# Performance work log

Measured on AMD Instinct MI355X. Metric: run time of the kernel, lower is better.

Reference implementation:

```python
import jax, jax.numpy as jnp
import numpy as np

B, L, D, H, P = 4, 4096, 1024, 8, 4
DPH = D // H


def _grid_sample_row(v, grid):
    """F.grid_sample for a (N, C, 1, Lv) input, bilinear, padding_mode='zeros',
    align_corners=False. v: (N, C, Lv), grid: (N, Lq, P, 2) with (x, y) in last dim.
    Returns (N, C, Lq, P)."""
    N, C, Lv = v.shape
    x = grid[..., 0]
    y = grid[..., 1]
    # unnormalize (align_corners=False): u = ((coord + 1) * size - 1) / 2
    ux = ((x + 1.0) * Lv - 1.0) * 0.5          # width = Lv
    uy = ((y + 1.0) * 1.0 - 1.0) * 0.5         # height = 1
    x0f = jnp.floor(ux)
    wx1 = ux - x0f
    wx0 = 1.0 - wx1
    y0f = jnp.floor(uy)
    wy1 = uy - y0f
    wy0 = 1.0 - wy1
    # only row 0 exists; rows outside contribute zero (padding zeros)
    wy = wy0 * (y0f == 0.0) + wy1 * ((y0f + 1.0) == 0.0)   # (N, Lq, P)
    i0 = x0f.astype(jnp.int32)
    i1 = i0 + 1
    m0 = (i0 >= 0) & (i0 < Lv)
    m1 = (i1 >= 0) & (i1 < Lv)
    i0c = jnp.clip(i0, 0, Lv - 1)
    i1c = jnp.clip(i1, 0, Lv - 1)
    # gather along width per batch element: (C, Lv)[:, (Lq, P)] -> (C, Lq, P)
    v0 = jax.vmap(lambda vv, ii: vv[:, ii])(v, i0c)
    v1 = jax.vmap(lambda vv, ii: vv[:, ii])(v, i1c)
    w0 = (wx0 * m0 * wy)[:, None, :, :]
    w1 = (wx1 * m1 * wy)[:, None, :, :]
    return v0 * w0 + v1 * w1


def setup_inputs() -> dict:
    key = jax.random.key(0)
    ks = jax.random.split(key, 16)
    s = 0.02
    f32 = jnp.float32
    return {
        "query": jax.random.normal(ks[0], (B, L, D), f32),
        "key_in": jax.random.normal(ks[1], (B, L, D), f32),
        "value": jax.random.normal(ks[2], (B, L, D), f32),
        "Wqk": jax.random.normal(ks[3], (D, 2 * D), f32) * s,
        "bqk": jnp.zeros((2 * D,), f32),
        "Wv": jax.random.normal(ks[4], (D, D), f32) * s,
        "bv": jnp.zeros((D,), f32),
        "Woff": jax.random.normal(ks[5], (D, H * P * 2), f32) * s,
        "boff": jax.random.normal(ks[6], (H * P * 2,), f32) * 0.25,
        "Wattn": jax.random.normal(ks[7], (D, H * P), f32) * s,
        "battn": jnp.zeros((H * P,), f32),
        "Wo": jax.random.normal(ks[8], (D, D), f32) * s,
        "bo": jnp.zeros((D,), f32),
    }


def reference(query, key_in, value, Wqk, bqk, Wv, bv, Woff, boff, Wattn, battn, Wo, bo):
    # qk_proj: q, k are computed in the original but never used downstream (dead code)
    qk = query @ Wqk + bqk
    q, k = jnp.split(qk, 2, axis=-1)  # noqa: unused, matches original

    v = value @ Wv + bv                                   # (B, L, D)

    # reference points: x base = linspace[0] = 0, y base = i/(L-1) for query i
    ref_y = jnp.linspace(0.0, 1.0, L)
    ref = jnp.stack([jnp.zeros_like(ref_y), ref_y], axis=-1)   # (L, 2)

    offsets = (query @ Woff + boff).reshape(B, L, H, P, 2)
    attn = jax.nn.softmax((query @ Wattn + battn).reshape(B, L, H, P), axis=-1)

    loc = jnp.clip(ref[None, :, None, None, :] + offsets, 0.0, 1.0)  # (B, L, H, P, 2)

    # value -> (B*H, dph, L)
    vh = v.reshape(B, L, H, DPH).transpose(0, 2, 3, 1).reshape(B * H, DPH, L)
    grid = loc.transpose(0, 2, 1, 3, 4).reshape(B * H, L, P, 2)

    sampled = _grid_sample_row(vh, grid)                  # (B*H, dph, L, P)
    sampled = sampled.reshape(B, H, DPH, L, P)

    aw = attn.transpose(0, 2, 1, 3)[:, :, None, :, :]     # (B, H, 1, L, P)
    out = (sampled * aw).sum(-1)                          # (B, H, dph, L)
    out = out.transpose(0, 3, 1, 2).reshape(B, L, D)
    return out @ Wo + bo
```

## Files before the change

kernel.cpp:

```cpp
#include <hip/hip_runtime.h>

#define L_Q 4096
#define D_MODEL 1024
#define N_B 4
#define N_H 8
#define N_P 4
#define M_ROWS (N_B * L_Q)

typedef float f32x4 __attribute__((ext_vector_type(4)));
typedef __bf16 bf16x8 __attribute__((ext_vector_type(8)));
typedef unsigned short u16x8 __attribute__((ext_vector_type(8)));

__device__ __forceinline__ unsigned short f2bf(float f) {
    unsigned int u = __float_as_uint(f);
    u += 0x7FFFu + ((u >> 16) & 1u);
    return (unsigned short)(u >> 16);
}
__device__ __forceinline__ float bf2f(unsigned short s) {
    return __uint_as_float(((unsigned int)s) << 16);
}

__device__ __forceinline__ void gload_lds16(const void* g, void* l) {
    __builtin_amdgcn_global_load_lds((const __attribute__((address_space(1))) void*)g,
                                     (__attribute__((address_space(3))) void*)l,
                                     16, 0, 0);
}

template <int N> __device__ __forceinline__ void wait_vmc() {
    if constexpr (N == 5)      asm volatile("s_waitcnt vmcnt(5)"  ::: "memory");
    else if constexpr (N == 4) asm volatile("s_waitcnt vmcnt(4)"  ::: "memory");
    else                       asm volatile("s_waitcnt vmcnt(0)"  ::: "memory");
}

#define RAW_BAR() asm volatile("s_barrier" ::: "memory")


__global__ void k_prep(const float* __restrict__ Wv, const float* __restrict__ Wo,
                       const float* __restrict__ Woff, const float* __restrict__ Wattn,
                       const float* __restrict__ value,
                       unsigned short* __restrict__ WvT, unsigned short* __restrict__ WoT,
                       unsigned short* __restrict__ WcT2, unsigned short* __restrict__ val_bf) {
    __shared__ float tile[64 * 65];
    const int bidx = blockIdx.x;
    const int t = threadIdx.x;

    if (bidx < 512) {
        const float* W = (bidx < 256) ? Wv : Wo;
        unsigned short* WT = (bidx < 256) ? WvT : WoT;
        const int bi = bidx & 255;
        const int k0 = (bi >> 4) * 64, n0 = (bi & 15) * 64;
#pragma unroll
        for (int j = 0; j < 4; ++j) {
            const int r = j * 16 + (t >> 4);
            float4 v = *(const float4*)(W + (size_t)(k0 + r) * 1024 + n0 + (t & 15) * 4);
            float* d = &tile[r * 65 + (t & 15) * 4];
            d[0] = v.x; d[1] = v.y; d[2] = v.z; d[3] = v.w;
        }
        __syncthreads();
#pragma unroll
        for (int j = 0; j < 4; ++j) {
            const int n = j * 16 + (t >> 4);
            const int kc = (t & 15) * 4;
            ushort4 o;
            o.x = f2bf(tile[(kc + 0) * 65 + n]);
            o.y = f2bf(tile[(kc + 1) * 65 + n]);
            o.z = f2bf(tile[(kc + 2) * 65 + n]);
            o.w = f2bf(tile[(kc + 3) * 65 + n]);
            *(ushort4*)(WT + (size_t)(n0 + n) * 1024 + k0 + kc) = o;
        }
    } else if (bidx < 544) {
        const int bi = bidx - 512;
        const int k0 = (bi >> 1) * 64;
        const int ntile = bi & 1;
        const int n0 = ntile * 64;
        const int nw = ntile ? 32 : 64;
        const int ldw = ntile ? 32 : 64;
        const float* W = ntile ? Wattn : Woff;
#pragma unroll
        for (int j = 0; j < 4; ++j) {
            const int r = j * 16 + (t >> 4);
            const int c4 = t & 15;
            if (c4 * 4 < nw) {
                float4 v = *(const float4*)(W + (size_t)(k0 + r) * ldw + c4 * 4);
                float* d = &tile[r * 65 + c4 * 4];
                d[0] = v.x; d[1] = v.y; d[2] = v.z; d[3] = v.w;
            }
        }
        __syncthreads();
#pragma unroll
        for (int j = 0; j < 4; ++j) {
            const int n = j * 16 + (t >> 4);
            if (n < nw) {
                const int kc = (t & 15) * 4;
                ushort4 hi, lo;
                float f0 = tile[(kc + 0) * 65 + n];
                float f1 = tile[(kc + 1) * 65 + n];
                float f2 = tile[(kc + 2) * 65 + n];
                float f3 = tile[(kc + 3) * 65 + n];
                hi.x = f2bf(f0); lo.x = f2bf(f0 - bf2f(hi.x));
                hi.y = f2bf(f1); lo.y = f2bf(f1 - bf2f(hi.y));
                hi.z = f2bf(f2); lo.z = f2bf(f2 - bf2f(hi.z));
                hi.w = f2bf(f3); lo.w = f2bf(f3 - bf2f(hi.w));
                const size_t base = (size_t)(n0 + n) * 2048 + k0 + kc;
                *(ushort4*)(WcT2 + base) = hi;
                *(ushort4*)(WcT2 + base + 1024) = lo;
            }
        }
    } else {
        const int n8 = M_ROWS * D_MODEL / 8;
        int i = (bidx - 544) * 256 + t;
        const int stride = (gridDim.x - 544) * 256;
        for (; i < n8; i += stride) {
            float4 a = ((const float4*)value)[2 * i];
            float4 b = ((const float4*)value)[2 * i + 1];
            u16x8 o;
            o[0] = f2bf(a.x); o[1] = f2bf(a.y); o[2] = f2bf(a.z); o[3] = f2bf(a.w);
            o[4] = f2bf(b.x); o[5] = f2bf(b.y); o[6] = f2bf(b.z); o[7] = f2bf(b.w);
            ((u16x8*)val_bf)[i] = o;
        }
    }
}


template <bool OUT_BF16>
__global__ __launch_bounds__(512, 2) void k_gemm256(const unsigned short* __restrict__ A,
                                                    const unsigned short* __restrict__ Bt,
                                                    const float* __restrict__ bias,
                                                    void* __restrict__ Cout) {
    __shared__ __align__(16) unsigned short lds[2][2][2][8192];
    const int tid = threadIdx.x;
    const int w = tid >> 6, lane = tid & 63;
    const int wm = w >> 2, wn = w & 3;

    const int bid = blockIdx.x;
    const int swz = (bid & 7) * 32 + (bid >> 3);
    const int m0 = (swz >> 2) * 256;
    const int n0 = (swz & 3) * 256;

    const int sr = (w << 3) + (lane >> 3);
    const int sc = (lane & 7) ^ ((lane >> 3) & 7);
    const size_t aoff1 = (size_t)(m0 + sr) * 1024 + (size_t)(sc * 8);
    const size_t boff1 = (size_t)(n0 + sr) * 1024 + (size_t)(sc * 8);

    const int fr = lane & 15, kq = lane >> 4;
    const int cs0 = ((kq) ^ (fr & 7)) * 8;
    const int cs1 = ((4 + kq) ^ (fr & 7)) * 8;
    const int arow = (wm * 64 + fr) * 64;
    const int brow = (wn * 32 + fr) * 64;

    f32x4 acc[2][2][4][2];
    const f32x4 zero = {0.f, 0.f, 0.f, 0.f};
#pragma unroll
    for (int qm = 0; qm < 2; ++qm)
#pragma unroll
        for (int qn = 0; qn < 2; ++qn)
#pragma unroll
            for (int i = 0; i < 4; ++i)
#pragma unroll
                for (int j = 0; j < 2; ++j) acc[qm][qn][i][j] = zero;

    bf16x8 af[4][2], bl[2][2], bh[2][2];

#define GSTA(set, half, kt) do {                                                        \
        const unsigned short* g_ = A + aoff1 + (size_t)(half) * 131072 + (size_t)(kt);  \
        unsigned short* d_ = &lds[0][set][half][0] + w * 512;                           \
        gload_lds16(g_, d_);                                                            \
        gload_lds16(g_ + 65536, d_ + 4096);                                             \
    } while (0)

#define GSTB(set, half, kt) do {                                                        \
        const unsigned short* g_ = Bt + boff1 + (size_t)(half) * 131072 + (size_t)(kt); \
        unsigned short* d_ = &lds[1][set][half][0] + w * 512;                           \
        gload_lds16(g_, d_);                                                            \
        gload_lds16(g_ + 65536, d_ + 4096);                                             \
    } while (0)

#define MFMA1(qm, qn, i, j, kk, B_)                                                     \
    acc[qm][qn][i][j] = __builtin_amdgcn_mfma_f32_16x16x32_bf16(                        \
        af[i][kk], B_[j][kk], acc[qm][qn][i][j], 0, 0, 0)

#define LDB4(dst, set, half) do {                                                       \
        const unsigned short* sB_ = &lds[1][set][half][0];                              \
        _Pragma("unroll") for (int j = 0; j < 2; ++j) {                                 \
            dst[j][0] = *(const bf16x8*)(sB_ + brow + j * 1024 + cs0);                  \
            dst[j][1] = *(const bf16x8*)(sB_ + brow + j * 1024 + cs1);                  \
        }                                                                               \
    } while (0)

#define LDA8(set, half) do {                                                            \
        const unsigned short* sA_ = &lds[0][set][half][0];                              \
        _Pragma("unroll") for (int i = 0; i < 4; ++i) {                                 \
            af[i][0] = *(const bf16x8*)(sA_ + arow + i * 1024 + cs0);                   \
            af[i][1] = *(const bf16x8*)(sA_ + arow + i * 1024 + cs1);                   \
        }                                                                               \
    } while (0)

#define MM16(qm, qn, B_) do {                                                           \
        _Pragma("unroll") for (int i = 0; i < 4; ++i) {                                 \
            MFMA1(qm, qn, i, 0, 0, B_); MFMA1(qm, qn, i, 0, 1, B_);                     \
            MFMA1(qm, qn, i, 1, 0, B_); MFMA1(qm, qn, i, 1, 1, B_);                     \
        }                                                                               \
    } while (0)

#define MM16_LDA(qm, qn, B_, setA, halfA) do {                                          \
        const unsigned short* sA_ = &lds[0][setA][halfA][0];                            \
        _Pragma("unroll") for (int i = 0; i < 4; ++i) {                                 \
            MFMA1(qm, qn, i, 0, 0, B_); MFMA1(qm, qn, i, 0, 1, B_);                     \
            MFMA1(qm, qn, i, 1, 0, B_); MFMA1(qm, qn, i, 1, 1, B_);                     \
            af[i][0] = *(const bf16x8*)(sA_ + arow + i * 1024 + cs0);                   \
            af[i][1] = *(const bf16x8*)(sA_ + arow + i * 1024 + cs1);                   \
        }                                                                               \
    } while (0)

#define SGB_MFMA(n) __builtin_amdgcn_sched_group_barrier(0x0008, n, 0)
#define SGB_DSR(n)  __builtin_amdgcn_sched_group_barrier(0x0100, n, 0)
#define PIN_A() do { SGB_DSR(4); SGB_MFMA(16); } while (0)
#define PIN_B() do { SGB_MFMA(4); SGB_DSR(2); SGB_MFMA(4); SGB_DSR(2);                  \
                     SGB_MFMA(4); SGB_DSR(2); SGB_MFMA(4); SGB_DSR(2); } while (0)
#define PIN_D() do { SGB_DSR(4); PIN_B(); } while (0)

    GSTA(0, 0, 0);
    GSTB(0, 0, 0);
    GSTB(0, 1, 0);
    GSTA(0, 1, 0);
    wait_vmc<4>();
    RAW_BAR();
    LDA8(0, 0); LDB4(bl, 0, 0);

#pragma unroll 1
    for (int it = 0; it < 8; ++it) {
        const int kt = it * 128;
        const int ktn = (kt + 128) & 1023;
        GSTA(1, 0, kt + 64);
        wait_vmc<4>(); RAW_BAR();
        __builtin_amdgcn_s_setprio(1);
        LDB4(bh, 0, 1);
        MM16(0, 0, bl);
        PIN_A();
        __builtin_amdgcn_s_setprio(0);
        GSTB(1, 0, kt + 64);
        wait_vmc<4>(); RAW_BAR();
        __builtin_amdgcn_s_setprio(1);
        MM16_LDA(0, 1, bh, 0, 1);
        PIN_B();
        __builtin_amdgcn_s_setprio(0);
        GSTB(1, 1, kt + 64);
        RAW_BAR();
        __builtin_amdgcn_s_setprio(1);
        MM16(1, 1, bh);
        __builtin_amdgcn_s_setprio(0);
        GSTA(1, 1, kt + 64);
        wait_vmc<4>(); RAW_BAR();
        __builtin_amdgcn_s_setprio(1);
        LDB4(bh, 1, 0);
        MM16_LDA(1, 0, bl, 1, 0);
        PIN_D();
        __builtin_amdgcn_s_setprio(0);
        GSTA(0, 0, ktn);
        wait_vmc<4>(); RAW_BAR();
        __builtin_amdgcn_s_setprio(1);
        LDB4(bl, 1, 1);
        MM16(0, 0, bh);
        PIN_A();
        __builtin_amdgcn_s_setprio(0);
        GSTB(0, 0, ktn);
        wait_vmc<4>(); RAW_BAR();
        __builtin_amdgcn_s_setprio(1);
        MM16_LDA(0, 1, bl, 1, 1);
        PIN_B();
        __builtin_amdgcn_s_setprio(0);
        GSTB(0, 1, ktn);
        RAW_BAR();
        __builtin_amdgcn_s_setprio(1);
        MM16(1, 1, bl);
        __builtin_amdgcn_s_setprio(0);
        GSTA(0, 1, ktn);
        wait_vmc<4>(); RAW_BAR();
        __builtin_amdgcn_s_setprio(1);
        LDB4(bl, 0, 0);
        MM16_LDA(1, 0, bh, 0, 0);
        PIN_D();
        __builtin_amdgcn_s_setprio(0);
    }
    wait_vmc<0>();

#undef GSTA
#undef GSTB
#undef MFMA1
#undef LDB4
#undef LDA8
#undef MM16
#undef MM16_LDA
#undef SGB_MFMA
#undef SGB_DSR
#undef PIN_A
#undef PIN_B
#undef PIN_D

#pragma unroll
    for (int qm = 0; qm < 2; ++qm) {
#pragma unroll
        for (int qn = 0; qn < 2; ++qn) {
#pragma unroll
            for (int i = 0; i < 4; ++i) {
#pragma unroll
                for (int j = 0; j < 2; ++j) {
                    const int col = n0 + qn * 128 + wn * 32 + j * 16 + fr;
                    const float bcol = bias[col];
#pragma unroll
                    for (int r = 0; r < 4; ++r) {
                        const int row = m0 + qm * 128 + wm * 64 + i * 16 + kq * 4 + r;
                        const float v = acc[qm][qn][i][j][r] + bcol;
                        if (OUT_BF16)
                            ((unsigned short*)Cout)[(size_t)row * D_MODEL + col] = f2bf(v);
                        else
                            ((float*)Cout)[(size_t)row * D_MODEL + col] = v;
                    }
                }
            }
        }
    }
}


__global__ __launch_bounds__(512, 2) void k_offattn2(const float* __restrict__ query,
                                                     const unsigned short* __restrict__ WcT2,
                                                     const float* __restrict__ boff,
                                                     const float* __restrict__ battn,
                                                     float* __restrict__ C96) {
    __shared__ __align__(16) unsigned short ldsA[2][128 * 64];
    __shared__ __align__(16) unsigned short ldsB[2][192 * 64];
    const int tid = threadIdx.x;
    const int w = tid >> 6, lane = tid & 63;
    const int wm = w >> 1, wn = w & 1;
    const int m0 = blockIdx.x * 64;

    const int ar = tid >> 3;
    const int ac = tid & 7;
    const float* qbase = query + (size_t)(m0 + ar) * 1024 + ac * 8;
    const int aw_hi = ar * 64 + ((ac ^ (ar & 7)) * 8);
    const int aw_lo = (64 + ar) * 64 + ((ac ^ (ar & 7)) * 8);

    const int brl = lane >> 3;
    const int bchk = (lane & 7) ^ (brl & 7);

    const int fr = lane & 15, kq = lane >> 4;
    const int cs0 = ((kq) ^ (fr & 7)) * 8;
    const int cs1 = ((4 + kq) ^ (fr & 7)) * 8;
    const int ahr = (wm * 16 + fr) * 64;
    const int alr = (64 + wm * 16 + fr) * 64;

    f32x4 acc[3];
    const f32x4 zero = {0.f, 0.f, 0.f, 0.f};
#pragma unroll
    for (int j = 0; j < 3; ++j) acc[j] = zero;

#define ALOAD(f0_, f1_, kt_) do {                                                       \
        f0_ = *(const float4*)(qbase + (kt_));                                          \
        f1_ = *(const float4*)(qbase + (kt_) + 4);                                      \
    } while (0)

#define BSTAGE(p_, kt_) do {                                                            \
        _Pragma("unroll") for (int i_ = 0; i_ < 3; ++i_) {                              \
            const int sr_ = i_ * 64 + w * 8 + brl;                                      \
            const unsigned short* g_ = WcT2 + ((sr_ < 96)                               \
                    ? ((size_t)sr_ * 2048 + (size_t)(kt_))                              \
                    : ((size_t)(sr_ - 96) * 2048 + 1024 + (size_t)(kt_)))               \
                    + (size_t)(bchk * 8);                                               \
            gload_lds16(g_, &ldsB[p_][(i_ * 64 + w * 8) * 64]);                         \
        }                                                                               \
    } while (0)

#define AWRITE2(p_, f0_, f1_) do {                                                      \
        u16x8 hi_, lo_;                                                                 \
        const float vv_[8] = {f0_.x, f0_.y, f0_.z, f0_.w, f1_.x, f1_.y, f1_.z, f1_.w};  \
        _Pragma("unroll") for (int e_ = 0; e_ < 8; ++e_) {                              \
            hi_[e_] = f2bf(vv_[e_]);                                                    \
            lo_[e_] = f2bf(vv_[e_] - bf2f(hi_[e_]));                                    \
        }                                                                               \
        *(u16x8*)(&ldsA[p_][aw_hi]) = hi_;                                              \
        *(u16x8*)(&ldsA[p_][aw_lo]) = lo_;                                              \
    } while (0)

#define OMM(p_) do {                                                                    \
        const unsigned short* As_ = &ldsA[p_][0];                                       \
        const unsigned short* Bs_ = &ldsB[p_][0];                                       \
        bf16x8 ah0 = *(const bf16x8*)(As_ + ahr + cs0);                                 \
        bf16x8 ah1 = *(const bf16x8*)(As_ + ahr + cs1);                                 \
        bf16x8 al0 = *(const bf16x8*)(As_ + alr + cs0);                                 \
        bf16x8 al1 = *(const bf16x8*)(As_ + alr + cs1);                                 \
        __builtin_amdgcn_s_setprio(1);                                                  \
        _Pragma("unroll") for (int j = 0; j < 3; ++j) {                                 \
            const int br_ = (wn * 48 + j * 16 + fr) * 64;                               \
            bf16x8 wh0 = *(const bf16x8*)(Bs_ + br_ + cs0);                             \
            bf16x8 wh1 = *(const bf16x8*)(Bs_ + br_ + cs1);                             \
            bf16x8 wl0 = *(const bf16x8*)(Bs_ + 6144 + br_ + cs0);                      \
            bf16x8 wl1 = *(const bf16x8*)(Bs_ + 6144 + br_ + cs1);                      \
            acc[j] = __builtin_amdgcn_mfma_f32_16x16x32_bf16(ah0, wh0, acc[j], 0, 0, 0);\
            acc[j] = __builtin_amdgcn_mfma_f32_16x16x32_bf16(ah1, wh1, acc[j], 0, 0, 0);\
            acc[j] = __builtin_amdgcn_mfma_f32_16x16x32_bf16(ah0, wl0, acc[j], 0, 0, 0);\
            acc[j] = __builtin_amdgcn_mfma_f32_16x16x32_bf16(ah1, wl1, acc[j], 0, 0, 0);\
            acc[j] = __builtin_amdgcn_mfma_f32_16x16x32_bf16(al0, wh0, acc[j], 0, 0, 0);\
            acc[j] = __builtin_amdgcn_mfma_f32_16x16x32_bf16(al1, wh1, acc[j], 0, 0, 0);\
        }                                                                               \
        __builtin_amdgcn_s_setprio(0);                                                  \
    } while (0)

#define OBODY(t_, p_, fc0_, fc1_, fn0_, fn1_) do {                                      \
        if ((t_) < 15) {                                                                \
            ALOAD(fn0_, fn1_, ((t_) + 1) * 64);                                         \
            BSTAGE((p_) ^ 1, ((t_) + 1) * 64);                                          \
            wait_vmc<5>();                                                              \
        } else {                                                                        \
            wait_vmc<0>();                                                              \
        }                                                                               \
        AWRITE2(p_, fc0_, fc1_);                                                        \
        asm volatile("s_waitcnt lgkmcnt(0)" ::: "memory");                              \
        RAW_BAR();                                                                      \
        OMM(p_);                                                                        \
        RAW_BAR();                                                                      \
    } while (0)

    float4 a0A, a1A, a0B, a1B;
    ALOAD(a0A, a1A, 0);
    BSTAGE(0, 0);

#pragma unroll 1
    for (int t2 = 0; t2 < 8; ++t2) {
        const int t = t2 * 2;
        OBODY(t,     0, a0A, a1A, a0B, a1B);
        OBODY(t + 1, 1, a0B, a1B, a0A, a1A);
    }

#undef ALOAD
#undef BSTAGE
#undef AWRITE2
#undef OMM
#undef OBODY

#pragma unroll
    for (int j = 0; j < 3; ++j) {
        const int col = wn * 48 + j * 16 + fr;
        const float bcol = (col < 64) ? boff[col] : battn[col - 64];
#pragma unroll
        for (int r = 0; r < 4; ++r) {
            const int row = m0 + wm * 16 + kq * 4 + r;
            C96[(size_t)row * 96 + col] = acc[j][r] + bcol;
        }
    }
}


__global__ void k_sampler(const float* __restrict__ C96,
                          const unsigned short* __restrict__ vproj,
                          unsigned short* __restrict__ agg) {
    const int row = blockIdx.x;
    const int b = row >> 12;
    const int l = row & (L_Q - 1);
    const int t = threadIdx.x;

    __shared__ float cv[96];
    if (t < 96) cv[t] = C96[(size_t)row * 96 + t];
    __syncthreads();

    const int h = t >> 5;
    const int dd = (t & 31) * 4;
    const float ref_y = (float)l / 4095.0f;

    float lg[4];
#pragma unroll
    for (int p = 0; p < 4; ++p) lg[p] = cv[64 + h * 4 + p];
    const float mx = fmaxf(fmaxf(lg[0], lg[1]), fmaxf(lg[2], lg[3]));
    float ex[4];
    float es = 0.f;
#pragma unroll
    for (int p = 0; p < 4; ++p) { ex[p] = expf(lg[p] - mx); es += ex[p]; }
    const float inv = 1.0f / es;

    float acc0 = 0.f, acc1 = 0.f, acc2 = 0.f, acc3 = 0.f;
#pragma unroll
    for (int p = 0; p < 4; ++p) {
        const float ox = cv[h * 8 + p * 2];
        const float oy = cv[h * 8 + p * 2 + 1];
        const float lx = fminf(fmaxf(ox, 0.0f), 1.0f);
        const float ly = fminf(fmaxf(ref_y + oy, 0.0f), 1.0f);
        const float ux = (lx + 1.0f) * 2048.0f - 0.5f;
        const float wy = 1.0f - ly * 0.5f;
        const float x0f = floorf(ux);
        const int i0 = (int)x0f;
        const int i1 = i0 + 1;
        const float w1 = ux - x0f;
        const float w0 = 1.0f - w1;
        const float aw = ex[p] * inv * wy;
        const float f0 = aw * w0 * ((i0 >= 0 && i0 < L_Q) ? 1.0f : 0.0f);
        const float f1 = aw * w1 * ((i1 >= 0 && i1 < L_Q) ? 1.0f : 0.0f);
        const int i0c = i0 < 0 ? 0 : (i0 > L_Q - 1 ? L_Q - 1 : i0);
        const int i1c = i1 < 0 ? 0 : (i1 > L_Q - 1 ? L_Q - 1 : i1);
        const ushort4 v0 = *(const ushort4*)(vproj + (size_t)(b * L_Q + i0c) * D_MODEL + h * 128 + dd);
        const ushort4 v1 = *(const ushort4*)(vproj + (size_t)(b * L_Q + i1c) * D_MODEL + h * 128 + dd);
        acc0 += f0 * bf2f(v0.x) + f1 * bf2f(v1.x);
        acc1 += f0 * bf2f(v0.y) + f1 * bf2f(v1.y);
        acc2 += f0 * bf2f(v0.z) + f1 * bf2f(v1.z);
        acc3 += f0 * bf2f(v0.w) + f1 * bf2f(v1.w);
    }
    ushort4 o;
    o.x = f2bf(acc0); o.y = f2bf(acc1); o.z = f2bf(acc2); o.w = f2bf(acc3);
    *(ushort4*)(agg + (size_t)row * D_MODEL + t * 4) = o;
}


extern "C" void kernel_launch(void* const* d_in, const int* in_sizes, int n_in,
                              void* d_out, int out_size, void* d_ws, size_t ws_size,
                              hipStream_t stream) {
    const float* query = (const float*)d_in[0];
    const float* value = (const float*)d_in[2];
    const float* Wv    = (const float*)d_in[5];
    const float* bv    = (const float*)d_in[6];
    const float* Woff  = (const float*)d_in[7];
    const float* boff  = (const float*)d_in[8];
    const float* Wattn = (const float*)d_in[9];
    const float* battn = (const float*)d_in[10];
    const float* Wo    = (const float*)d_in[11];
    const float* bo    = (const float*)d_in[12];

    char* ws = (char*)d_ws;
    size_t off = 0;
    auto alloc = [&](size_t bytes) -> char* {
        char* p = ws + off;
        off += (bytes + 255) & ~(size_t)255;
        return p;
    };
    unsigned short* val_bf = (unsigned short*)alloc((size_t)M_ROWS * D_MODEL * 2);
    unsigned short* vproj  = (unsigned short*)alloc((size_t)M_ROWS * D_MODEL * 2);
    unsigned short* agg    = (unsigned short*)alloc((size_t)M_ROWS * D_MODEL * 2);
    float*          C96    = (float*)alloc((size_t)M_ROWS * 96 * 4);
    unsigned short* WvT    = (unsigned short*)alloc((size_t)D_MODEL * D_MODEL * 2);
    unsigned short* WoT    = (unsigned short*)alloc((size_t)D_MODEL * D_MODEL * 2);
    unsigned short* WcT2   = (unsigned short*)alloc((size_t)96 * 2048 * 2);

    k_prep<<<2048, 256, 0, stream>>>(Wv, Wo, Woff, Wattn, value, WvT, WoT, WcT2, val_bf);

    k_gemm256<true><<<256, 512, 0, stream>>>(val_bf, WvT, bv, vproj);

    k_offattn2<<<M_ROWS / 64, 512, 0, stream>>>(query, WcT2, boff, battn, C96);

    k_sampler<<<M_ROWS, 256, 0, stream>>>(C96, vproj, agg);

    k_gemm256<false><<<256, 512, 0, stream>>>(agg, WoT, bo, (float*)d_out);
}
```

Before: 142.8 us.

## Fuse offset/attention projection with bilinear sampler via shared memory

Merges the offset/attention-logit GEMM kernel and the sampler kernel into one. The 96-column projection results stay in LDS instead of going through a global C96 buffer, and each 512-thread block then samples its 64 rows in a loop. This removes one kernel launch and the global write and read of the intermediate. The cost is that the sampling phase now runs inside a heavier GEMM block with higher LDS use, so fewer sampler blocks are resident to hide gather latency.

```diff
diff --git a/kernel.cpp b/kernel.cpp
--- a/kernel.cpp
+++ b/kernel.cpp
@@ -323,11 +323,12 @@
 }
 
 
-__global__ __launch_bounds__(512, 2) void k_offattn2(const float* __restrict__ query,
-                                                     const unsigned short* __restrict__ WcT2,
-                                                     const float* __restrict__ boff,
-                                                     const float* __restrict__ battn,
-                                                     float* __restrict__ C96) {
+__global__ __launch_bounds__(512, 2) void k_offsamp(const float* __restrict__ query,
+                                                    const unsigned short* __restrict__ WcT2,
+                                                    const float* __restrict__ boff,
+                                                    const float* __restrict__ battn,
+                                                    const unsigned short* __restrict__ vproj,
+                                                    unsigned short* __restrict__ agg) {
     __shared__ __align__(16) unsigned short ldsA[2][128 * 64];
     __shared__ __align__(16) unsigned short ldsB[2][192 * 64];
     const int tid = threadIdx.x;
@@ -438,74 +439,74 @@
 #undef OMM
 #undef OBODY
 
+    asm volatile("s_waitcnt lgkmcnt(0)" ::: "memory");
+    __syncthreads();
+
+    float* cvs = (float*)&ldsA[0][0];
 #pragma unroll
     for (int j = 0; j < 3; ++j) {
         const int col = wn * 48 + j * 16 + fr;
         const float bcol = (col < 64) ? boff[col] : battn[col - 64];
 #pragma unroll
         for (int r = 0; r < 4; ++r) {
-            const int row = m0 + wm * 16 + kq * 4 + r;
-            C96[(size_t)row * 96 + col] = acc[j][r] + bcol;
+            const int rl = wm * 16 + kq * 4 + r;
+            cvs[rl * 96 + col] = acc[j][r] + bcol;
         }
     }
-}
-
-
-__global__ void k_sampler(const float* __restrict__ C96,
-                          const unsigned short* __restrict__ vproj,
-                          unsigned short* __restrict__ agg) {
-    const int row = blockIdx.x;
-    const int b = row >> 12;
-    const int l = row & (L_Q - 1);
-    const int t = threadIdx.x;
-
-    __shared__ float cv[96];
-    if (t < 96) cv[t] = C96[(size_t)row * 96 + t];
     __syncthreads();
 
-    const int h = t >> 5;
-    const int dd = (t & 31) * 4;
-    const float ref_y = (float)l / 4095.0f;
-
-    float lg[4];
-#pragma unroll
-    for (int p = 0; p < 4; ++p) lg[p] = cv[64 + h * 4 + p];
-    const float mx = fmaxf(fmaxf(lg[0], lg[1]), fmaxf(lg[2], lg[3]));
-    float ex[4];
-    float es = 0.f;
-#pragma unroll
-    for (int p = 0; p < 4; ++p) { ex[p] = expf(lg[p] - mx); es += ex[p]; }
-    const float inv = 1.0f / es;
-
-    float acc0 = 0.f, acc1 = 0.f, acc2 = 0.f, acc3 = 0.f;
-#pragma unroll
-    for (int p = 0; p < 4; ++p) {
-        const float ox = cv[h * 8 + p * 2];
-        const float oy = cv[h * 8 + p * 2 + 1];
-        const float lx = fminf(fmaxf(ox, 0.0f), 1.0f);
-        const float ly = fminf(fmaxf(ref_y + oy, 0.0f), 1.0f);
-        const float ux = (lx + 1.0f) * 2048.0f - 0.5f;
-        const float wy = 1.0f - ly * 0.5f;
-        const float x0f = floorf(ux);
-        const int i0 = (int)x0f;
-        const int i1 = i0 + 1;
-        const float w1 = ux - x0f;
-        const float w0 = 1.0f - w1;
-        const float aw = ex[p] * inv * wy;
-        const float f0 = aw * w0 * ((i0 >= 0 && i0 < L_Q) ? 1.0f : 0.0f);
-        const float f1 = aw * w1 * ((i1 >= 0 && i1 < L_Q) ? 1.0f : 0.0f);
-        const int i0c = i0 < 0 ? 0 : (i0 > L_Q - 1 ? L_Q - 1 : i0);
-        const int i1c = i1 < 0 ? 0 : (i1 > L_Q - 1 ? L_Q - 1 : i1);
-        const ushort4 v0 = *(const ushort4*)(vproj + (size_t)(b * L_Q + i0c) * D_MODEL + h * 128 + dd);
-        const ushort4 v1 = *(const ushort4*)(vproj + (size_t)(b * L_Q + i1c) * D_MODEL + h * 128 + dd);
-        acc0 += f0 * bf2f(v0.x) + f1 * bf2f(v1.x);
-        acc1 += f0 * bf2f(v0.y) + f1 * bf2f(v1.y);
-        acc2 += f0 * bf2f(v0.z) + f1 * bf2f(v1.z);
-        acc3 += f0 * bf2f(v0.w) + f1 * bf2f(v1.w);
+    const int b = m0 >> 12;
+#pragma unroll 2
+    for (int rep = 0; rep < 32; ++rep) {
+        const int task = rep * 512 + tid;
+        const int rl = task >> 8;
+        const int ct = task & 255;
+        const int l = (m0 + rl) & (L_Q - 1);
+        const int h = ct >> 5;
+        const int dd = (ct & 31) * 4;
+        const float ref_y = (float)l / 4095.0f;
+        const float* cv = &cvs[rl * 96];
+
+        float lg[4];
+#pragma unroll
+        for (int p = 0; p < 4; ++p) lg[p] = cv[64 + h * 4 + p];
+        const float mx = fmaxf(fmaxf(lg[0], lg[1]), fmaxf(lg[2], lg[3]));
+        float ex[4];
+        float es = 0.f;
+#pragma unroll
+        for (int p = 0; p < 4; ++p) { ex[p] = expf(lg[p] - mx); es += ex[p]; }
+        const float inv = 1.0f / es;
+
+        float acc0 = 0.f, acc1 = 0.f, acc2 = 0.f, acc3 = 0.f;
+#pragma unroll
+        for (int p = 0; p < 4; ++p) {
+            const float ox = cv[h * 8 + p * 2];
+            const float oy = cv[h * 8 + p * 2 + 1];
+            const float lx = fminf(fmaxf(ox, 0.0f), 1.0f);
+            const float ly = fminf(fmaxf(ref_y + oy, 0.0f), 1.0f);
+            const float ux = (lx + 1.0f) * 2048.0f - 0.5f;
+            const float wy = 1.0f - ly * 0.5f;
+            const float x0f = floorf(ux);
+            const int i0 = (int)x0f;
+            const int i1 = i0 + 1;
+            const float w1 = ux - x0f;
+            const float w0 = 1.0f - w1;
+            const float aw = ex[p] * inv * wy;
+            const float f0 = aw * w0 * ((i0 >= 0 && i0 < L_Q) ? 1.0f : 0.0f);
+            const float f1 = aw * w1 * ((i1 >= 0 && i1 < L_Q) ? 1.0f : 0.0f);
+            const int i0c = i0 < 0 ? 0 : (i0 > L_Q - 1 ? L_Q - 1 : i0);
+            const int i1c = i1 < 0 ? 0 : (i1 > L_Q - 1 ? L_Q - 1 : i1);
+            const ushort4 v0 = *(const ushort4*)(vproj + (size_t)(b * L_Q + i0c) * D_MODEL + h * 128 + dd);
+            const ushort4 v1 = *(const ushort4*)(vproj + (size_t)(b * L_Q + i1c) * D_MODEL + h * 128 + dd);
+            acc0 += f0 * bf2f(v0.x) + f1 * bf2f(v1.x);
+            acc1 += f0 * bf2f(v0.y) + f1 * bf2f(v1.y);
+            acc2 += f0 * bf2f(v0.z) + f1 * bf2f(v1.z);
+            acc3 += f0 * bf2f(v0.w) + f1 * bf2f(v1.w);
+        }
+        ushort4 o;
+        o.x = f2bf(acc0); o.y = f2bf(acc1); o.z = f2bf(acc2); o.w = f2bf(acc3);
+        *(ushort4*)(agg + (size_t)(m0 + rl) * D_MODEL + ct * 4) = o;
     }
-    ushort4 o;
-    o.x = f2bf(acc0); o.y = f2bf(acc1); o.z = f2bf(acc2); o.w = f2bf(acc3);
-    *(ushort4*)(agg + (size_t)row * D_MODEL + t * 4) = o;
 }
 
 
@@ -533,7 +534,6 @@
     unsigned short* val_bf = (unsigned short*)alloc((size_t)M_ROWS * D_MODEL * 2);
     unsigned short* vproj  = (unsigned short*)alloc((size_t)M_ROWS * D_MODEL * 2);
     unsigned short* agg    = (unsigned short*)alloc((size_t)M_ROWS * D_MODEL * 2);
-    float*          C96    = (float*)alloc((size_t)M_ROWS * 96 * 4);
     unsigned short* WvT    = (unsigned short*)alloc((size_t)D_MODEL * D_MODEL * 2);
     unsigned short* WoT    = (unsigned short*)alloc((size_t)D_MODEL * D_MODEL * 2);
     unsigned short* WcT2   = (unsigned short*)alloc((size_t)96 * 2048 * 2);
@@ -542,9 +542,7 @@
 
     k_gemm256<true><<<256, 512, 0, stream>>>(val_bf, WvT, bv, vproj);
 
-    k_offattn2<<<M_ROWS / 64, 512, 0, stream>>>(query, WcT2, boff, battn, C96);
-
-    k_sampler<<<M_ROWS, 256, 0, stream>>>(C96, vproj, agg);
+    k_offsamp<<<M_ROWS / 64, 512, 0, stream>>>(query, WcT2, boff, battn, vproj, agg);
 
     k_gemm256<false><<<256, 512, 0, stream>>>(agg, WoT, bo, (float*)d_out);
 }
```

Result: slower. 157.1 us (+10.0%).
